# Performance work log

Hardware: AMD Instinct MI355X
Metric: run time of the kernel (lower is better)

Reference implementation:

```python
import jax, jax.numpy as jnp
import numpy as np

L, H, HM, E = 2, 1024, 256, 64  # layers, hidden, hyper hidden, hyper embedding
B, T, D = 64, 256, 1024         # batch, time, input size (D == H so layers stack)


def setup_inputs() -> dict:
    key = jax.random.key(0)
    ks = jax.random.split(key, 16)
    n = jax.random.normal
    inp = {
        'x':   n(ks[0], (B, T, D), jnp.float32),
        # main LSTM weights: 4 gates (i,f,g,o); last dim is the input dim
        'Wx':  n(ks[1], (L, 4, H, D), jnp.float32) / np.sqrt(D),
        'Wh':  n(ks[2], (L, 4, H, H), jnp.float32) / np.sqrt(H),
        # hyper (meta) LSTM: input is concat(x_t, h) of size D+H
        'Wmx': n(ks[3], (L, 4 * HM, D + H), jnp.float32) / np.sqrt(D + H),
        'Wmh': n(ks[4], (L, 4 * HM, HM), jnp.float32) / np.sqrt(HM),
        'bm':  jnp.zeros((L, 4 * HM), jnp.float32),
        # hyper embeddings z per gate (hidden->4xE projections)
        'Wzx': n(ks[5], (L, HM, 4, E), jnp.float32) / np.sqrt(HM),
        'bzx': jnp.ones((L, 4, E), jnp.float32),
        'Wzh': n(ks[6], (L, HM, 4, E), jnp.float32) / np.sqrt(HM),
        'bzh': jnp.ones((L, 4, E), jnp.float32),
        'Wzb': n(ks[7], (L, HM, 4, E), jnp.float32) / np.sqrt(HM),
        # embedding -> per-unit modulation (E->H per gate)
        'Px':  n(ks[8], (L, 4, E, H), jnp.float32) / np.sqrt(E),
        'Ph':  n(ks[9], (L, 4, E, H), jnp.float32) / np.sqrt(E),
        'Pb':  n(ks[10], (L, 4, E, H), jnp.float32) / np.sqrt(E),
    }
    return inp


def _meta_lstm_forward(x, Wx, Wh, Wmx, Wmh, bm, Wzx, bzx, Wzh, bzh, Wzb, Px, Ph, Pb):
    Bb = x.shape[0]
    inp = x
    for l in range(L):
        def step(carry, xt, l=l):
            h, c, mh, mc = carry
            # hyper LSTM step on concat(x_t, h)
            xcat = jnp.concatenate([xt, h], axis=-1)
            mpre = xcat @ Wmx[l].T + mh @ Wmh[l].T + bm[l]
            mi, mf, mg, mo = jnp.split(mpre, 4, axis=-1)
            mc2 = jax.nn.sigmoid(mf) * mc + jax.nn.sigmoid(mi) * jnp.tanh(mg)
            mh2 = jax.nn.sigmoid(mo) * jnp.tanh(mc2)
            # gate embeddings and per-unit modulation vectors [B,4,H]
            zx = jnp.einsum('bm,mge->bge', mh2, Wzx[l]) + bzx[l]
            zh = jnp.einsum('bm,mge->bge', mh2, Wzh[l]) + bzh[l]
            zb = jnp.einsum('bm,mge->bge', mh2, Wzb[l])
            dx = jnp.einsum('bge,geh->bgh', zx, Px[l])
            dh = jnp.einsum('bge,geh->bgh', zh, Ph[l])
            db = jnp.einsum('bge,geh->bgh', zb, Pb[l])
            # main LSTM gate pre-activations, hyper-modulated
            gx = jnp.einsum('bd,ghd->bgh', xt, Wx[l])
            gh = jnp.einsum('bk,ghk->bgh', h, Wh[l])
            pre = dx * gx + dh * gh + db
            i_, f_, g_, o_ = pre[:, 0], pre[:, 1], pre[:, 2], pre[:, 3]
            c2 = jax.nn.sigmoid(f_) * c + jax.nn.sigmoid(i_) * jnp.tanh(g_)
            h2 = jax.nn.sigmoid(o_) * jnp.tanh(c2)
            return (h2, c2, mh2, mc2), h2
        init = (jnp.zeros((Bb, H), x.dtype), jnp.zeros((Bb, H), x.dtype),
                jnp.zeros((Bb, HM), x.dtype), jnp.zeros((Bb, HM), x.dtype))
        xs = jnp.swapaxes(inp, 0, 1)  # [T,B,D]
        _, hs = jax.lax.scan(step, init, xs)
        inp = jnp.swapaxes(hs, 0, 1)  # [B,T,H]
    return inp


def reference(x, Wx, Wh, Wmx, Wmh, bm, Wzx, bzx, Wzh, bzh, Wzb, Px, Ph, Pb):
    return _meta_lstm_forward(x, Wx, Wh, Wmx, Wmh, bm, Wzx, bzx, Wzh, bzh, Wzb, Px, Ph, Pb)
```

## Files before the change

### kernel.cpp

```cpp
#include <hip/hip_runtime.h>
#include <hip/hip_cooperative_groups.h>

namespace cg = cooperative_groups;

#define Bb 64
#define Tt 256
#define Dd 1024
#define Hh 1024
#define HMm 256
#define Ee 64

__device__ __forceinline__ float b2f(unsigned short u){
    union{unsigned int i; float f;} v; v.i = ((unsigned int)u) << 16; return v.f;
}
__device__ __forceinline__ unsigned short f2bf(float f){
    union{float f; unsigned int i;} v; v.f = f;
    unsigned int x = v.i;
    unsigned int r = (x + 0x7fffu + ((x >> 16) & 1u)) >> 16;
    return (unsigned short)r;
}
__device__ __forceinline__ void up2(unsigned int u, float& lo, float& hi){
    union{unsigned int i; float f;} x, y;
    x.i = u << 16; y.i = u & 0xffff0000u; lo = x.f; hi = y.f;
}
__device__ __forceinline__ float sigf(float x){ return 1.f/(1.f + expf(-x)); }

__device__ __forceinline__ float ldT(const unsigned short* p){ return b2f(*p); }
__device__ __forceinline__ float ldT(const float* p){ return *p; }
__device__ __forceinline__ void stT(unsigned short* p, float v){ *p = f2bf(v); }
__device__ __forceinline__ void stT(float* p, float v){ *p = v; }

__device__ __forceinline__ void ld8(const unsigned short* p, float* f){
    uint4 u = *(const uint4*)(const void*)p;
    up2(u.x,f[0],f[1]); up2(u.y,f[2],f[3]); up2(u.z,f[4],f[5]); up2(u.w,f[6],f[7]);
}
__device__ __forceinline__ void ld8(const float* p, float* f){
    float4 a = *(const float4*)(const void*)p;
    float4 b = *(const float4*)(const void*)(p+4);
    f[0]=a.x; f[1]=a.y; f[2]=a.z; f[3]=a.w; f[4]=b.x; f[5]=b.y; f[6]=b.z; f[7]=b.w;
}
__device__ __forceinline__ float dot8(const float* a, const float* b, float acc){
    #pragma unroll
    for(int i=0;i<8;i++) acc += a[i]*b[i];
    return acc;
}

__global__ void k_detect(const unsigned short* __restrict__ x, int* __restrict__ flag){
    int tid = threadIdx.x;
    float v = fabsf(b2f(x[2 * tid]));
    bool in = (v > 1e-4f) && (v < 50.f);
    unsigned long long m = __ballot(in);
    if(tid == 0) *flag = (__popcll(m) >= 32) ? 0 : 1;
}

__global__ __launch_bounds__(1024, 4) void coop_rnn_bf16(
    const unsigned short* x,
    const unsigned short* __restrict__ Wx, const unsigned short* __restrict__ Wh,
    const unsigned short* __restrict__ Wmx, const unsigned short* __restrict__ Wmh,
    const unsigned short* __restrict__ bm,
    const unsigned short* __restrict__ Wzx, const unsigned short* __restrict__ bzx,
    const unsigned short* __restrict__ Wzh, const unsigned short* __restrict__ bzh,
    const unsigned short* __restrict__ Wzb,
    const unsigned short* __restrict__ Px, const unsigned short* __restrict__ Ph,
    const unsigned short* __restrict__ Pb,
    unsigned short* out, float* ws, const int* flag)
{
    if(*flag != 0) return;
    cg::grid_group grid = cg::this_grid();

    float* h0   = ws;
    float* h1   = ws + 65536;
    float* cst  = ws + 131072;
    float* m0   = ws + 196608;
    float* m1   = ws + 212992;
    float* mcst = ws + 229376;
    float* z    = ws + 245760;
    unsigned short* xbuf16 = (unsigned short*)(ws + 294912);

    int tid = threadIdx.x, bid = blockIdx.x;

    __shared__ __align__(16) unsigned short sWx[16][4][264];
    __shared__ __align__(16) unsigned short sWh[16][4][264];
    __shared__ __align__(16) unsigned short sWmxX[4][4][264];
    __shared__ __align__(16) unsigned short sWmxH[4][4][264];
    __shared__ __align__(16) unsigned short sWmh[4][4][72];
    __shared__ __align__(16) unsigned short sWz[3][4][72];
    __shared__ __align__(16) unsigned short sP[3][4][64][4];
    __shared__ float sBm[4], sBz[2];
    __shared__ float sA[256];
    __shared__ float spre[1024];

    for(int l = 0; l < 2; l++){
        const unsigned short* xseq = l ? out : x;
        const unsigned short* Wx_l  = Wx  + (size_t)l * 4194304;
        const unsigned short* Wh_l  = Wh  + (size_t)l * 4194304;
        const unsigned short* Wmx_l = Wmx + (size_t)l * 2097152;
        const unsigned short* Wmh_l = Wmh + (size_t)l * 262144;
        const unsigned short* bm_l  = bm  + l * 1024;
        const unsigned short* Wz0 = Wzx + l * 65536;
        const unsigned short* Wz1 = Wzh + l * 65536;
        const unsigned short* Wz2 = Wzb + l * 65536;
        const unsigned short* bz0 = bzx + l * 256;
        const unsigned short* bz1 = bzh + l * 256;
        const unsigned short* Px_l = Px + l * 262144;
        const unsigned short* Ph_l = Ph + l * 262144;
        const unsigned short* Pb_l = Pb + l * 262144;

        {
            int gid = bid * 1024 + tid;
            if(gid < 65536){ h0[gid] = 0.f; cst[gid] = 0.f; }
            if(gid < 16384){ m0[gid] = 0.f; mcst[gid] = 0.f; }
        }

        for(int idx = tid; idx < 16384; idx += 1024){
            int rr = idx >> 10, k = idx & 1023;
            int g = rr >> 2, hh = rr & 3;
            size_t n = (size_t)(g * 1024 + bid * 4 + hh);
            sWx[rr][k >> 8][k & 255] = Wx_l[n * 1024 + k];
        }
        for(int idx = tid; idx < 16384; idx += 1024){
            int rr = idx >> 10, k = idx & 1023;
            int g = rr >> 2, hh = rr & 3;
            size_t n = (size_t)(g * 1024 + bid * 4 + hh);
            sWh[rr][k >> 8][k & 255] = Wh_l[n * 1024 + k];
        }
        for(int idx = tid; idx < 4096; idx += 1024){
            int r = idx >> 10, k = idx & 1023;
            size_t row = (size_t)(r * 256 + bid);
            sWmxX[r][k >> 8][k & 255] = Wmx_l[row * 2048 + k];
            sWmxH[r][k >> 8][k & 255] = Wmx_l[row * 2048 + 1024 + k];
        }
        {
            int r = tid >> 8, m = tid & 255;
            sWmh[r][m >> 6][m & 63] = Wmh_l[(size_t)(r * 256 + bid) * 256 + m];
        }
        if(tid < 768){
            int s_ = tid >> 8, m = tid & 255;
            const unsigned short* W = (s_ == 0) ? Wz0 : ((s_ == 1) ? Wz1 : Wz2);
            sWz[s_][m >> 6][m & 63] = W[m * 256 + bid];
        }
        {
            int g = tid >> 8, e = (tid >> 2) & 63, hh = tid & 3;
            int pi = (g * 64 + e) * 1024 + bid * 4 + hh;
            sP[0][g][e][hh] = Px_l[pi];
            sP[1][g][e][hh] = Ph_l[pi];
            sP[2][g][e][hh] = Pb_l[pi];
        }
        if(tid < 4) sBm[tid] = ldT(&bm_l[tid * 256 + bid]);
        if(tid == 4) sBz[0] = ldT(&bz0[bid]);
        if(tid == 5) sBz[1] = ldT(&bz1[bid]);

        float *hp = h0, *hn = h1, *mp = m0, *mn = m1;
        grid.sync();

        for(int t = 0; t < 256; t++){
            {
                int sg = bid * 1024 + tid;
                if(sg < 65536){
                    int xb = sg >> 10, xd = sg & 1023;
                    xbuf16[sg] = xseq[((size_t)xb * Tt + t) * Dd + xd];
                }

                int r  = tid >> 8;
                int b  = (tid >> 2) & 63;
                int ks = tid & 3;
                const unsigned short* wxp = &sWmxX[r][ks][0];
                const unsigned short* whp_ = &sWmxH[r][ks][0];
                const unsigned short* wmp = &sWmh[r][ks][0];
                const unsigned short* xr = xseq + ((size_t)b * Tt + t) * Dd + ks * 256;
                const float* hr = hp + b * 1024 + ks * 256;
                const float* mr = mp + b * 256 + ks * 64;
                float a0 = 0.f, a1 = 0.f, a2 = 0.f, a3 = 0.f;
                float wf[8], vf[8];
                for(int k = 0; k < 256; k += 16){
                    ld8(wxp + k, wf);     ld8(xr + k, vf);     a0 = dot8(wf, vf, a0);
                    ld8(wxp + k + 8, wf); ld8(xr + k + 8, vf); a1 = dot8(wf, vf, a1);
                }
                for(int k = 0; k < 256; k += 16){
                    ld8(whp_ + k, wf);     ld8(hr + k, vf);     a2 = dot8(wf, vf, a2);
                    ld8(whp_ + k + 8, wf); ld8(hr + k + 8, vf); a3 = dot8(wf, vf, a3);
                }
                for(int m = 0; m < 64; m += 16){
                    ld8(wmp + m, wf);     ld8(mr + m, vf);     a0 = dot8(wf, vf, a0);
                    ld8(wmp + m + 8, wf); ld8(mr + m + 8, vf); a1 = dot8(wf, vf, a1);
                }
                float a = (a0 + a1) + (a2 + a3);
                a += __shfl_xor(a, 1);
                a += __shfl_xor(a, 2);
                if(ks == 0) sA[r * 64 + b] = a + sBm[r];
            }
            __syncthreads();
            if(tid < 64){
                int b = tid;
                float mi = sA[b], mf = sA[64 + b], mg = sA[128 + b], mo = sA[192 + b];
                int idx = b * 256 + bid;
                float mc2 = sigf(mf) * mcst[idx] + sigf(mi) * tanhf(mg);
                mcst[idx] = mc2;
                mn[idx] = sigf(mo) * tanhf(mc2);
            }
            grid.sync();

            if(tid < 768){
                int s_ = tid >> 8, sub = tid & 255;
                int b = sub >> 2, ks = sub & 3;
                const unsigned short* wz = &sWz[s_][ks][0];
                const float* mr = mn + b * 256 + ks * 64;
                float acc = 0.f; float wf[8], vf[8];
                for(int m = 0; m < 64; m += 16){
                    ld8(wz + m, wf);     ld8(mr + m, vf);     acc = dot8(wf, vf, acc);
                    ld8(wz + m + 8, wf); ld8(mr + m + 8, vf); acc = dot8(wf, vf, acc);
                }
                acc += __shfl_xor(acc, 1);
                acc += __shfl_xor(acc, 2);
                if(ks == 0){
                    float biasv = (s_ == 0) ? sBz[0] : ((s_ == 1) ? sBz[1] : 0.f);
                    z[((s_ * 256) + bid) * 64 + b] = acc + biasv;
                }
            }
            grid.sync();

            {
                int r16 = tid >> 6;
                int g = r16 >> 2, hh = r16 & 3;
                int bg = (tid >> 2) & 15;
                int ks = tid & 3;
                int b0 = bg * 4;
                const unsigned short* wxr = &sWx[r16][ks][0];
                const unsigned short* whr = &sWh[r16][ks][0];
                float gx[4] = {0,0,0,0}, gh[4] = {0,0,0,0};
                for(int k = 0; k < 256; k += 8){
                    float wf[8]; ld8(wxr + k, wf);
                    #pragma unroll
                    for(int i = 0; i < 4; i++){
                        float xf[8]; ld8(xbuf16 + (b0 + i) * 1024 + ks * 256 + k, xf);
                        gx[i] = dot8(wf, xf, gx[i]);
                    }
                }
                for(int k = 0; k < 256; k += 8){
                    float wf[8]; ld8(whr + k, wf);
                    #pragma unroll
                    for(int i = 0; i < 4; i++){
                        float hf[8]; ld8(hp + (b0 + i) * 1024 + ks * 256 + k, hf);
                        gh[i] = dot8(wf, hf, gh[i]);
                    }
                }
                float dx[4] = {0,0,0,0}, dh[4] = {0,0,0,0}, db[4] = {0,0,0,0};
                int e0 = ks * 16;
                for(int e = e0; e < e0 + 16; e++){
                    int zc = g * 64 + e;
                    float pxv = b2f(sP[0][g][e][hh]);
                    float phv = b2f(sP[1][g][e][hh]);
                    float pbv = b2f(sP[2][g][e][hh]);
                    const float4 zx4 = *(const float4*)&z[(0 * 256 + zc) * 64 + b0];
                    const float4 zh4 = *(const float4*)&z[(1 * 256 + zc) * 64 + b0];
                    const float4 zb4 = *(const float4*)&z[(2 * 256 + zc) * 64 + b0];
                    dx[0] += zx4.x * pxv; dx[1] += zx4.y * pxv; dx[2] += zx4.z * pxv; dx[3] += zx4.w * pxv;
                    dh[0] += zh4.x * phv; dh[1] += zh4.y * phv; dh[2] += zh4.z * phv; dh[3] += zh4.w * phv;
                    db[0] += zb4.x * pbv; db[1] += zb4.y * pbv; db[2] += zb4.z * pbv; db[3] += zb4.w * pbv;
                }
                #pragma unroll
                for(int i = 0; i < 4; i++){
                    gx[i] += __shfl_xor(gx[i], 1); gx[i] += __shfl_xor(gx[i], 2);
                    gh[i] += __shfl_xor(gh[i], 1); gh[i] += __shfl_xor(gh[i], 2);
                    dx[i] += __shfl_xor(dx[i], 1); dx[i] += __shfl_xor(dx[i], 2);
                    dh[i] += __shfl_xor(dh[i], 1); dh[i] += __shfl_xor(dh[i], 2);
                    db[i] += __shfl_xor(db[i], 1); db[i] += __shfl_xor(db[i], 2);
                }
                if(ks == 0){
                    #pragma unroll
                    for(int i = 0; i < 4; i++)
                        spre[r16 * 64 + b0 + i] = dx[i] * gx[i] + dh[i] * gh[i] + db[i];
                }
            }
            __syncthreads();
            if(tid < 256){
                int hh = tid >> 6, b = tid & 63;
                float pi_ = spre[(0 * 4 + hh) * 64 + b];
                float pf_ = spre[(1 * 4 + hh) * 64 + b];
                float pg_ = spre[(2 * 4 + hh) * 64 + b];
                float po_ = spre[(3 * 4 + hh) * 64 + b];
                int h = bid * 4 + hh;
                int idx = b * 1024 + h;
                float c2 = sigf(pf_) * cst[idx] + sigf(pi_) * tanhf(pg_);
                float h2 = sigf(po_) * tanhf(c2);
                cst[idx] = c2;
                hn[idx] = h2;
                stT(&out[((size_t)b * Tt + t) * Dd + h], h2);
            }
            grid.sync();

            float* tp = hp; hp = hn; hn = tp;
            tp = mp; mp = mn; mn = tp;
        }
    }
}

__global__ __launch_bounds__(1024, 4) void coop_rnn_f32(
    const float* x,
    const float* __restrict__ Wx, const float* __restrict__ Wh,
    const float* __restrict__ Wmx, const float* __restrict__ Wmh, const float* __restrict__ bm,
    const float* __restrict__ Wzx, const float* __restrict__ bzx,
    const float* __restrict__ Wzh, const float* __restrict__ bzh, const float* __restrict__ Wzb,
    const float* __restrict__ Px, const float* __restrict__ Ph, const float* __restrict__ Pb,
    float* out, float* ws, const int* flag)
{
    if(*flag != 1) return;
    cg::grid_group grid = cg::this_grid();

    float* h0   = ws;
    float* h1   = ws + 65536;
    float* cst  = ws + 131072;
    float* m0   = ws + 196608;
    float* m1   = ws + 212992;
    float* mcst = ws + 229376;
    float* z    = ws + 245760;
    float* xbuf = ws + 294912;

    int tid = threadIdx.x, bid = blockIdx.x;

    __shared__ __align__(16) float sWx[16][4][264];
    __shared__ __align__(16) float sWh[16][4][264];
    __shared__ __align__(16) float sP[3][4][64][5];
    __shared__ float sA[256];
    __shared__ float spre[1024];

    for(int l = 0; l < 2; l++){
        const float* xseq = l ? out : x;
        const float* Wx_l  = Wx  + (size_t)l * 4194304;
        const float* Wh_l  = Wh  + (size_t)l * 4194304;
        const float* Wmx_l = Wmx + (size_t)l * 2097152;
        const float* Wmh_l = Wmh + (size_t)l * 262144;
        const float* bm_l  = bm  + l * 1024;
        const float* Wz0 = Wzx + l * 65536;
        const float* Wz1 = Wzh + l * 65536;
        const float* Wz2 = Wzb + l * 65536;
        const float* bz0 = bzx + l * 256;
        const float* bz1 = bzh + l * 256;
        const float* Px_l = Px + l * 262144;
        const float* Ph_l = Ph + l * 262144;
        const float* Pb_l = Pb + l * 262144;

        {
            int gid = bid * 1024 + tid;
            if(gid < 65536){ h0[gid] = 0.f; cst[gid] = 0.f; }
            if(gid < 16384){ m0[gid] = 0.f; mcst[gid] = 0.f; }
        }

        for(int idx = tid; idx < 16384; idx += 1024){
            int rr = idx >> 10, k = idx & 1023;
            int g = rr >> 2, hh = rr & 3;
            size_t n = (size_t)(g * 1024 + bid * 4 + hh);
            sWx[rr][k >> 8][k & 255] = Wx_l[n * 1024 + k];
            sWh[rr][k >> 8][k & 255] = Wh_l[n * 1024 + k];
        }
        {
            int g = tid >> 8, e = (tid >> 2) & 63, hh = tid & 3;
            int pi = (g * 64 + e) * 1024 + bid * 4 + hh;
            sP[0][g][e][hh] = Px_l[pi];
            sP[1][g][e][hh] = Ph_l[pi];
            sP[2][g][e][hh] = Pb_l[pi];
        }

        float *hp = h0, *hn = h1, *mp = m0, *mn = m1;
        grid.sync();

        for(int t = 0; t < 256; t++){
            {
                int sg = bid * 1024 + tid;
                if(sg < 65536){
                    int xb = sg >> 10, xd = sg & 1023;
                    xbuf[sg] = ldT(&xseq[((size_t)xb * Tt + t) * Dd + xd]);
                }
                int r  = tid >> 8;
                int b  = (tid >> 2) & 63;
                int ks = tid & 3;
                int row = r * 256 + bid;
                const float* wr = Wmx_l + (size_t)row * 2048;
                const float* wm = Wmh_l + (size_t)row * 256;
                const float* xr = xseq + ((size_t)b * Tt + t) * Dd;
                const float* hr = hp + b * 1024;
                const float* mr = mp + b * 256;
                float a0 = 0.f, a1 = 0.f, a2 = 0.f, a3 = 0.f;
                float wf[8], vf[8];
                int k0 = ks * 256;
                for(int k = k0; k < k0 + 256; k += 16){
                    ld8(wr + k, wf);      ld8(xr + k, vf);      a0 = dot8(wf, vf, a0);
                    ld8(wr + k + 8, wf);  ld8(xr + k + 8, vf);  a1 = dot8(wf, vf, a1);
                }
                for(int k = k0; k < k0 + 256; k += 16){
                    ld8(wr + 1024 + k, wf);     ld8(hr + k, vf);     a2 = dot8(wf, vf, a2);
                    ld8(wr + 1024 + k + 8, wf); ld8(hr + k + 8, vf); a3 = dot8(wf, vf, a3);
                }
                int ms = ks * 64;
                for(int m = ms; m < ms + 64; m += 16){
                    ld8(wm + m, wf);     ld8(mr + m, vf);     a0 = dot8(wf, vf, a0);
                    ld8(wm + m + 8, wf); ld8(mr + m + 8, vf); a1 = dot8(wf, vf, a1);
                }
                float a = (a0 + a1) + (a2 + a3);
                a += __shfl_xor(a, 1);
                a += __shfl_xor(a, 2);
                if(ks == 0) sA[r * 64 + b] = a + ldT(&bm_l[row]);
            }
            __syncthreads();
            if(tid < 64){
                int b = tid;
                float mi = sA[b], mf = sA[64 + b], mg = sA[128 + b], mo = sA[192 + b];
                int idx = b * 256 + bid;
                float mc2 = sigf(mf) * mcst[idx] + sigf(mi) * tanhf(mg);
                mcst[idx] = mc2;
                mn[idx] = sigf(mo) * tanhf(mc2);
            }
            grid.sync();

            if(bid < 192){
                int s_ = bid >> 6, b = bid & 63;
                int ks = tid >> 8, col = tid & 255;
                const float* W = (s_ == 0) ? Wz0 : ((s_ == 1) ? Wz1 : Wz2);
                const float* mr = mn + b * 256;
                float acc = 0.f;
                int ms = ks * 64;
                #pragma unroll 8
                for(int m = ms; m < ms + 64; m++)
                    acc += mr[m] * ldT(&W[m * 256 + col]);
                spre[tid] = acc;
                __syncthreads();
                if(tid < 256){
                    float biasv = (s_ == 0) ? ldT(&bz0[tid]) : ((s_ == 1) ? ldT(&bz1[tid]) : 0.f);
                    z[(s_ * 64 + b) * 256 + tid] =
                        biasv + ((spre[tid] + spre[256 + tid]) + (spre[512 + tid] + spre[768 + tid]));
                }
            }
            grid.sync();

            {
                int r16 = tid >> 6;
                int g = r16 >> 2, hh = r16 & 3;
                int bg = (tid >> 2) & 15;
                int ks = tid & 3;
                int b0 = bg * 4;
                const float* wxr = &sWx[r16][ks][0];
                const float* whr = &sWh[r16][ks][0];
                float gx[4] = {0,0,0,0}, gh[4] = {0,0,0,0};
                for(int k = 0; k < 256; k += 8){
                    float wf[8]; ld8(wxr + k, wf);
                    #pragma unroll
                    for(int i = 0; i < 4; i++){
                        float xf[8]; ld8(xbuf + (b0 + i) * 1024 + ks * 256 + k, xf);
                        gx[i] = dot8(wf, xf, gx[i]);
                    }
                }
                for(int k = 0; k < 256; k += 8){
                    float wf[8]; ld8(whr + k, wf);
                    #pragma unroll
                    for(int i = 0; i < 4; i++){
                        float hf[8]; ld8(hp + (b0 + i) * 1024 + ks * 256 + k, hf);
                        gh[i] = dot8(wf, hf, gh[i]);
                    }
                }
                float dx[4] = {0,0,0,0}, dh[4] = {0,0,0,0}, db[4] = {0,0,0,0};
                int e0 = ks * 16;
                for(int e = e0; e < e0 + 16; e++){
                    float pxv = sP[0][g][e][hh];
                    float phv = sP[1][g][e][hh];
                    float pbv = sP[2][g][e][hh];
                    int zc = g * 64 + e;
                    #pragma unroll
                    for(int i = 0; i < 4; i++){
                        int b = b0 + i;
                        dx[i] += z[(b) * 256 + zc] * pxv;
                        dh[i] += z[(64 + b) * 256 + zc] * phv;
                        db[i] += z[(128 + b) * 256 + zc] * pbv;
                    }
                }
                #pragma unroll
                for(int i = 0; i < 4; i++){
                    gx[i] += __shfl_xor(gx[i], 1); gx[i] += __shfl_xor(gx[i], 2);
                    gh[i] += __shfl_xor(gh[i], 1); gh[i] += __shfl_xor(gh[i], 2);
                    dx[i] += __shfl_xor(dx[i], 1); dx[i] += __shfl_xor(dx[i], 2);
                    dh[i] += __shfl_xor(dh[i], 1); dh[i] += __shfl_xor(dh[i], 2);
                    db[i] += __shfl_xor(db[i], 1); db[i] += __shfl_xor(db[i], 2);
                }
                if(ks == 0){
                    #pragma unroll
                    for(int i = 0; i < 4; i++)
                        spre[r16 * 64 + b0 + i] = dx[i] * gx[i] + dh[i] * gh[i] + db[i];
                }
            }
            __syncthreads();
            if(tid < 256){
                int hh = tid >> 6, b = tid & 63;
                float pi_ = spre[(0 * 4 + hh) * 64 + b];
                float pf_ = spre[(1 * 4 + hh) * 64 + b];
                float pg_ = spre[(2 * 4 + hh) * 64 + b];
                float po_ = spre[(3 * 4 + hh) * 64 + b];
                int h = bid * 4 + hh;
                int idx = b * 1024 + h;
                float c2 = sigf(pf_) * cst[idx] + sigf(pi_) * tanhf(pg_);
                float h2 = sigf(po_) * tanhf(c2);
                cst[idx] = c2;
                hn[idx] = h2;
                stT(&out[((size_t)b * Tt + t) * Dd + h], h2);
            }
            grid.sync();

            float* tp = hp; hp = hn; hn = tp;
            tp = mp; mp = mn; mn = tp;
        }
    }
}

static void launch_bf16(void* const* d_in, void* d_out, float* ws, int* flag, hipStream_t stream){
    const unsigned short* xp   = (const unsigned short*)d_in[0];
    const unsigned short* Wxp  = (const unsigned short*)d_in[1];
    const unsigned short* Whp  = (const unsigned short*)d_in[2];
    const unsigned short* Wmxp = (const unsigned short*)d_in[3];
    const unsigned short* Wmhp = (const unsigned short*)d_in[4];
    const unsigned short* bmp  = (const unsigned short*)d_in[5];
    const unsigned short* Wzxp = (const unsigned short*)d_in[6];
    const unsigned short* bzxp = (const unsigned short*)d_in[7];
    const unsigned short* Wzhp = (const unsigned short*)d_in[8];
    const unsigned short* bzhp = (const unsigned short*)d_in[9];
    const unsigned short* Wzbp = (const unsigned short*)d_in[10];
    const unsigned short* Pxp  = (const unsigned short*)d_in[11];
    const unsigned short* Php  = (const unsigned short*)d_in[12];
    const unsigned short* Pbp  = (const unsigned short*)d_in[13];
    unsigned short* outp = (unsigned short*)d_out;
    void* args[] = {
        (void*)&xp, (void*)&Wxp, (void*)&Whp, (void*)&Wmxp, (void*)&Wmhp, (void*)&bmp,
        (void*)&Wzxp, (void*)&bzxp, (void*)&Wzhp, (void*)&bzhp, (void*)&Wzbp,
        (void*)&Pxp, (void*)&Php, (void*)&Pbp, (void*)&outp, (void*)&ws, (void*)&flag
    };
    hipLaunchCooperativeKernel((void*)coop_rnn_bf16, dim3(256), dim3(1024), args, 0, stream);
}

static void launch_f32(void* const* d_in, void* d_out, float* ws, int* flag, hipStream_t stream){
    const float* xp   = (const float*)d_in[0];
    const float* Wxp  = (const float*)d_in[1];
    const float* Whp  = (const float*)d_in[2];
    const float* Wmxp = (const float*)d_in[3];
    const float* Wmhp = (const float*)d_in[4];
    const float* bmp  = (const float*)d_in[5];
    const float* Wzxp = (const float*)d_in[6];
    const float* bzxp = (const float*)d_in[7];
    const float* Wzhp = (const float*)d_in[8];
    const float* bzhp = (const float*)d_in[9];
    const float* Wzbp = (const float*)d_in[10];
    const float* Pxp  = (const float*)d_in[11];
    const float* Php  = (const float*)d_in[12];
    const float* Pbp  = (const float*)d_in[13];
    float* outp = (float*)d_out;
    void* args[] = {
        (void*)&xp, (void*)&Wxp, (void*)&Whp, (void*)&Wmxp, (void*)&Wmhp, (void*)&bmp,
        (void*)&Wzxp, (void*)&bzxp, (void*)&Wzhp, (void*)&bzhp, (void*)&Wzbp,
        (void*)&Pxp, (void*)&Php, (void*)&Pbp, (void*)&outp, (void*)&ws, (void*)&flag
    };
    hipLaunchCooperativeKernel((void*)coop_rnn_f32, dim3(256), dim3(1024), args, 0, stream);
}

extern "C" void kernel_launch(void* const* d_in, const int* in_sizes, int n_in,
                              void* d_out, int out_size, void* d_ws, size_t ws_size,
                              hipStream_t stream) {
    (void)in_sizes; (void)n_in; (void)out_size; (void)ws_size;
    float* ws = (float*)d_ws;
    int* flag = (int*)(ws + 360448);

    k_detect<<<1, 64, 0, stream>>>((const unsigned short*)d_in[0], flag);
    launch_bf16(d_in, d_out, ws, flag, stream);
    launch_f32(d_in, d_out, ws, flag, stream);
}
```

Measured before the change: 252.8 ms.

## Replace cooperative grid.sync with custom atomic barrier and cache hyper-z weights in LDS

Result: slower. 681.1 ms (+169.4%).

```diff
diff --git a/kernel.cpp b/kernel.cpp
--- a/kernel.cpp
+++ b/kernel.cpp
@@ -45,12 +45,53 @@
     return acc;
 }
 
-__global__ void k_detect(const unsigned short* __restrict__ x, int* __restrict__ flag){
+__device__ __forceinline__ float ld_c(const float* p){
+    return __hip_atomic_load(p, __ATOMIC_RELAXED, __HIP_MEMORY_SCOPE_AGENT);
+}
+__device__ __forceinline__ void st_c(float* p, float v){
+    __hip_atomic_store(p, v, __ATOMIC_RELAXED, __HIP_MEMORY_SCOPE_AGENT);
+}
+__device__ __forceinline__ void ld2_c(const float* p, float* f){
+    union{unsigned long long u; float fv[2];} c;
+    c.u = __hip_atomic_load((const unsigned long long*)(const void*)p,
+                            __ATOMIC_RELAXED, __HIP_MEMORY_SCOPE_AGENT);
+    f[0] = c.fv[0]; f[1] = c.fv[1];
+}
+__device__ __forceinline__ void ld4_c(const float* p, float* f){
+    ld2_c(p, f); ld2_c(p + 2, f + 2);
+}
+__device__ __forceinline__ void ld8_c(const float* p, float* f){
+    ld2_c(p, f); ld2_c(p + 2, f + 2); ld2_c(p + 4, f + 4); ld2_c(p + 6, f + 6);
+}
+
+__device__ __forceinline__ void gbar(unsigned* cnt, unsigned* gen, int nb){
+    __syncthreads();
+    if(threadIdx.x == 0){
+        asm volatile("" ::: "memory");
+        unsigned g = __hip_atomic_load(gen, __ATOMIC_RELAXED, __HIP_MEMORY_SCOPE_AGENT);
+        unsigned a = __hip_atomic_fetch_add(cnt, 1u, __ATOMIC_RELEASE, __HIP_MEMORY_SCOPE_AGENT);
+        if(a == (unsigned)(nb - 1)){
+            __hip_atomic_store(cnt, 0u, __ATOMIC_RELAXED, __HIP_MEMORY_SCOPE_AGENT);
+            __hip_atomic_store(gen, g + 1u, __ATOMIC_RELEASE, __HIP_MEMORY_SCOPE_AGENT);
+        }else{
+            while(__hip_atomic_load(gen, __ATOMIC_RELAXED, __HIP_MEMORY_SCOPE_AGENT) == g)
+                __builtin_amdgcn_s_sleep(32);
+        }
+        asm volatile("" ::: "memory");
+    }
+    __syncthreads();
+}
+
+__global__ void k_detect(const unsigned short* __restrict__ x, int* __restrict__ flag,
+                         unsigned* __restrict__ cnt, unsigned* __restrict__ gen){
     int tid = threadIdx.x;
     float v = fabsf(b2f(x[2 * tid]));
     bool in = (v > 1e-4f) && (v < 50.f);
     unsigned long long m = __ballot(in);
-    if(tid == 0) *flag = (__popcll(m) >= 32) ? 0 : 1;
+    if(tid == 0){
+        *flag = (__popcll(m) >= 32) ? 0 : 1;
+        *cnt = 0u; *gen = 0u;
+    }
 }
 
 __global__ __launch_bounds__(1024, 4) void coop_rnn_bf16(
@@ -302,10 +343,9 @@
     const float* __restrict__ Wzx, const float* __restrict__ bzx,
     const float* __restrict__ Wzh, const float* __restrict__ bzh, const float* __restrict__ Wzb,
     const float* __restrict__ Px, const float* __restrict__ Ph, const float* __restrict__ Pb,
-    float* out, float* ws, const int* flag)
+    float* out, float* ws, const int* flag, unsigned* bcnt, unsigned* bgen)
 {
     if(*flag != 1) return;
-    cg::grid_group grid = cg::this_grid();
 
     float* h0   = ws;
     float* h1   = ws + 65536;
@@ -321,6 +361,7 @@
     __shared__ __align__(16) float sWx[16][4][264];
     __shared__ __align__(16) float sWh[16][4][264];
     __shared__ __align__(16) float sP[3][4][64][5];
+    __shared__ __align__(16) float sWz[3][4][68];
     __shared__ float sA[256];
     __shared__ float spre[1024];
 
@@ -342,8 +383,8 @@
 
         {
             int gid = bid * 1024 + tid;
-            if(gid < 65536){ h0[gid] = 0.f; cst[gid] = 0.f; }
-            if(gid < 16384){ m0[gid] = 0.f; mcst[gid] = 0.f; }
+            if(gid < 65536){ st_c(&h0[gid], 0.f); st_c(&cst[gid], 0.f); }
+            if(gid < 16384){ st_c(&m0[gid], 0.f); st_c(&mcst[gid], 0.f); }
         }
 
         for(int idx = tid; idx < 16384; idx += 1024){
@@ -360,16 +401,21 @@
             sP[1][g][e][hh] = Ph_l[pi];
             sP[2][g][e][hh] = Pb_l[pi];
         }
+        if(tid < 768){
+            int s_ = tid >> 8, m = tid & 255;
+            const float* W = (s_ == 0) ? Wz0 : ((s_ == 1) ? Wz1 : Wz2);
+            sWz[s_][m >> 6][m & 63] = W[m * 256 + bid];
+        }
 
         float *hp = h0, *hn = h1, *mp = m0, *mn = m1;
-        grid.sync();
+        gbar(bcnt, bgen, 256);
 
         for(int t = 0; t < 256; t++){
             {
                 int sg = bid * 1024 + tid;
                 if(sg < 65536){
                     int xb = sg >> 10, xd = sg & 1023;
-                    xbuf[sg] = ldT(&xseq[((size_t)xb * Tt + t) * Dd + xd]);
+                    st_c(&xbuf[sg], ld_c(&xseq[((size_t)xb * Tt + t) * Dd + xd]));
                 }
                 int r  = tid >> 8;
                 int b  = (tid >> 2) & 63;
@@ -384,17 +430,17 @@
                 float wf[8], vf[8];
                 int k0 = ks * 256;
                 for(int k = k0; k < k0 + 256; k += 16){
-                    ld8(wr + k, wf);      ld8(xr + k, vf);      a0 = dot8(wf, vf, a0);
-                    ld8(wr + k + 8, wf);  ld8(xr + k + 8, vf);  a1 = dot8(wf, vf, a1);
+                    ld8(wr + k, wf);      ld8_c(xr + k, vf);      a0 = dot8(wf, vf, a0);
+                    ld8(wr + k + 8, wf);  ld8_c(xr + k + 8, vf);  a1 = dot8(wf, vf, a1);
                 }
                 for(int k = k0; k < k0 + 256; k += 16){
-                    ld8(wr + 1024 + k, wf);     ld8(hr + k, vf);     a2 = dot8(wf, vf, a2);
-                    ld8(wr + 1024 + k + 8, wf); ld8(hr + k + 8, vf); a3 = dot8(wf, vf, a3);
+                    ld8(wr + 1024 + k, wf);     ld8_c(hr + k, vf);     a2 = dot8(wf, vf, a2);
+                    ld8(wr + 1024 + k + 8, wf); ld8_c(hr + k + 8, vf); a3 = dot8(wf, vf, a3);
                 }
                 int ms = ks * 64;
                 for(int m = ms; m < ms + 64; m += 16){
-                    ld8(wm + m, wf);     ld8(mr + m, vf);     a0 = dot8(wf, vf, a0);
-                    ld8(wm + m + 8, wf); ld8(mr + m + 8, vf); a1 = dot8(wf, vf, a1);
+                    ld8(wm + m, wf);     ld8_c(mr + m, vf);     a0 = dot8(wf, vf, a0);
+                    ld8(wm + m + 8, wf); ld8_c(mr + m + 8, vf); a1 = dot8(wf, vf, a1);
                 }
                 float a = (a0 + a1) + (a2 + a3);
                 a += __shfl_xor(a, 1);
@@ -406,31 +452,30 @@
                 int b = tid;
                 float mi = sA[b], mf = sA[64 + b], mg = sA[128 + b], mo = sA[192 + b];
                 int idx = b * 256 + bid;
-                float mc2 = sigf(mf) * mcst[idx] + sigf(mi) * tanhf(mg);
-                mcst[idx] = mc2;
-                mn[idx] = sigf(mo) * tanhf(mc2);
-            }
-            grid.sync();
-
-            if(bid < 192){
-                int s_ = bid >> 6, b = bid & 63;
-                int ks = tid >> 8, col = tid & 255;
-                const float* W = (s_ == 0) ? Wz0 : ((s_ == 1) ? Wz1 : Wz2);
-                const float* mr = mn + b * 256;
-                float acc = 0.f;
-                int ms = ks * 64;
-                #pragma unroll 8
-                for(int m = ms; m < ms + 64; m++)
-                    acc += mr[m] * ldT(&W[m * 256 + col]);
-                spre[tid] = acc;
-                __syncthreads();
-                if(tid < 256){
-                    float biasv = (s_ == 0) ? ldT(&bz0[tid]) : ((s_ == 1) ? ldT(&bz1[tid]) : 0.f);
-                    z[(s_ * 64 + b) * 256 + tid] =
-                        biasv + ((spre[tid] + spre[256 + tid]) + (spre[512 + tid] + spre[768 + tid]));
-                }
-            }
-            grid.sync();
+                float mc2 = sigf(mf) * ld_c(&mcst[idx]) + sigf(mi) * tanhf(mg);
+                st_c(&mcst[idx], mc2);
+                st_c(&mn[idx], sigf(mo) * tanhf(mc2));
+            }
+            gbar(bcnt, bgen, 256);
+
+            if(tid < 768){
+                int s_ = tid >> 8, sub = tid & 255;
+                int b = sub >> 2, ks = sub & 3;
+                const float* wz = &sWz[s_][ks][0];
+                const float* mr = mn + b * 256 + ks * 64;
+                float acc = 0.f; float wf[8], vf[8];
+                for(int m = 0; m < 64; m += 16){
+                    ld8(wz + m, wf);     ld8_c(mr + m, vf);     acc = dot8(wf, vf, acc);
+                    ld8(wz + m + 8, wf); ld8_c(mr + m + 8, vf); acc = dot8(wf, vf, acc);
+                }
+                acc += __shfl_xor(acc, 1);
+                acc += __shfl_xor(acc, 2);
+                if(ks == 0){
+                    float biasv = (s_ == 0) ? ldT(&bz0[bid]) : ((s_ == 1) ? ldT(&bz1[bid]) : 0.f);
+                    st_c(&z[((s_ * 256) + bid) * 64 + b], acc + biasv);
+                }
+            }
+            gbar(bcnt, bgen, 256);
 
             {
                 int r16 = tid >> 6;
@@ -445,7 +490,7 @@
                     float wf[8]; ld8(wxr + k, wf);
                     #pragma unroll
                     for(int i = 0; i < 4; i++){
-                        float xf[8]; ld8(xbuf + (b0 + i) * 1024 + ks * 256 + k, xf);
+                        float xf[8]; ld8_c(xbuf + (b0 + i) * 1024 + ks * 256 + k, xf);
                         gx[i] = dot8(wf, xf, gx[i]);
                     }
                 }
@@ -453,23 +498,26 @@
                     float wf[8]; ld8(whr + k, wf);
                     #pragma unroll
                     for(int i = 0; i < 4; i++){
-                        float hf[8]; ld8(hp + (b0 + i) * 1024 + ks * 256 + k, hf);
+                        float hf[8]; ld8_c(hp + (b0 + i) * 1024 + ks * 256 + k, hf);
                         gh[i] = dot8(wf, hf, gh[i]);
                     }
                 }
                 float dx[4] = {0,0,0,0}, dh[4] = {0,0,0,0}, db[4] = {0,0,0,0};
                 int e0 = ks * 16;
                 for(int e = e0; e < e0 + 16; e++){
+                    int zc = g * 64 + e;
                     float pxv = sP[0][g][e][hh];
                     float phv = sP[1][g][e][hh];
                     float pbv = sP[2][g][e][hh];
-                    int zc = g * 64 + e;
+                    float zx4[4], zh4[4], zb4[4];
+                    ld4_c(&z[(0 * 256 + zc) * 64 + b0], zx4);
+                    ld4_c(&z[(1 * 256 + zc) * 64 + b0], zh4);
+                    ld4_c(&z[(2 * 256 + zc) * 64 + b0], zb4);
                     #pragma unroll
                     for(int i = 0; i < 4; i++){
-                        int b = b0 + i;
-                        dx[i] += z[(b) * 256 + zc] * pxv;
-                        dh[i] += z[(64 + b) * 256 + zc] * phv;
-                        db[i] += z[(128 + b) * 256 + zc] * pbv;
+                        dx[i] += zx4[i] * pxv;
+                        dh[i] += zh4[i] * phv;
+                        db[i] += zb4[i] * pbv;
                     }
                 }
                 #pragma unroll
@@ -495,13 +543,13 @@
                 float po_ = spre[(3 * 4 + hh) * 64 + b];
                 int h = bid * 4 + hh;
                 int idx = b * 1024 + h;
-                float c2 = sigf(pf_) * cst[idx] + sigf(pi_) * tanhf(pg_);
+                float c2 = sigf(pf_) * ld_c(&cst[idx]) + sigf(pi_) * tanhf(pg_);
                 float h2 = sigf(po_) * tanhf(c2);
-                cst[idx] = c2;
-                hn[idx] = h2;
-                stT(&out[((size_t)b * Tt + t) * Dd + h], h2);
-            }
-            grid.sync();
+                st_c(&cst[idx], c2);
+                st_c(&hn[idx], h2);
+                st_c(&out[((size_t)b * Tt + t) * Dd + h], h2);
+            }
+            gbar(bcnt, bgen, 256);
 
             float* tp = hp; hp = hn; hn = tp;
             tp = mp; mp = mn; mn = tp;
@@ -533,7 +581,8 @@
     hipLaunchCooperativeKernel((void*)coop_rnn_bf16, dim3(256), dim3(1024), args, 0, stream);
 }
 
-static void launch_f32(void* const* d_in, void* d_out, float* ws, int* flag, hipStream_t stream){
+static void launch_f32(void* const* d_in, void* d_out, float* ws, int* flag,
+                       unsigned* bcnt, unsigned* bgen, hipStream_t stream){
     const float* xp   = (const float*)d_in[0];
     const float* Wxp  = (const float*)d_in[1];
     const float* Whp  = (const float*)d_in[2];
@@ -552,7 +601,8 @@
     void* args[] = {
         (void*)&xp, (void*)&Wxp, (void*)&Whp, (void*)&Wmxp, (void*)&Wmhp, (void*)&bmp,
         (void*)&Wzxp, (void*)&bzxp, (void*)&Wzhp, (void*)&bzhp, (void*)&Wzbp,
-        (void*)&Pxp, (void*)&Php, (void*)&Pbp, (void*)&outp, (void*)&ws, (void*)&flag
+        (void*)&Pxp, (void*)&Php, (void*)&Pbp, (void*)&outp, (void*)&ws, (void*)&flag,
+        (void*)&bcnt, (void*)&bgen
     };
     hipLaunchCooperativeKernel((void*)coop_rnn_f32, dim3(256), dim3(1024), args, 0, stream);
 }
@@ -563,8 +613,10 @@
     (void)in_sizes; (void)n_in; (void)out_size; (void)ws_size;
     float* ws = (float*)d_ws;
     int* flag = (int*)(ws + 360448);
-
-    k_detect<<<1, 64, 0, stream>>>((const unsigned short*)d_in[0], flag);
+    unsigned* bcnt = (unsigned*)(ws + 360464);
+    unsigned* bgen = (unsigned*)(ws + 360480);
+
+    k_detect<<<1, 64, 0, stream>>>((const unsigned short*)d_in[0], flag, bcnt, bgen);
     launch_bf16(d_in, d_out, ws, flag, stream);
-    launch_f32(d_in, d_out, ws, flag, stream);
-}
+    launch_f32(d_in, d_out, ws, flag, bcnt, bgen, stream);
+}
```

## Restructure f32 cooperative RNN: register-resident hyper weights, hoisted main-gate GEMV, 512 threads

Applied to the files above, without the earlier changes.

Result: faster. 235.7 ms (-6.8%).

```diff
diff --git a/kernel.cpp b/kernel.cpp
--- a/kernel.cpp
+++ b/kernel.cpp
@@ -43,6 +43,11 @@
     #pragma unroll
     for(int i=0;i<8;i++) acc += a[i]*b[i];
     return acc;
+}
+__device__ __forceinline__ float redsum64(float s){
+    #pragma unroll
+    for(int o = 1; o < 64; o <<= 1) s += __shfl_xor(s, o);
+    return s;
 }
 
 __global__ void k_detect(const unsigned short* __restrict__ x, int* __restrict__ flag){
@@ -160,7 +165,6 @@
                     int xb = sg >> 10, xd = sg & 1023;
                     xbuf16[sg] = xseq[((size_t)xb * Tt + t) * Dd + xd];
                 }
-
                 int r  = tid >> 8;
                 int b  = (tid >> 2) & 63;
                 int ks = tid & 3;
@@ -295,7 +299,7 @@
     }
 }
 
-__global__ __launch_bounds__(1024, 4) void coop_rnn_f32(
+__global__ __launch_bounds__(512, 2) void coop_rnn_f32(
     const float* x,
     const float* __restrict__ Wx, const float* __restrict__ Wh,
     const float* __restrict__ Wmx, const float* __restrict__ Wmh, const float* __restrict__ bm,
@@ -314,15 +318,18 @@
     float* m1   = ws + 212992;
     float* mcst = ws + 229376;
     float* z    = ws + 245760;
-    float* xbuf = ws + 294912;
 
     int tid = threadIdx.x, bid = blockIdx.x;
-
-    __shared__ __align__(16) float sWx[16][4][264];
-    __shared__ __align__(16) float sWh[16][4][264];
-    __shared__ __align__(16) float sP[3][4][64][5];
-    __shared__ float sA[256];
+    int wave = tid >> 6, lane = tid & 63;
+
+    __shared__ __align__(16) float sWx[16][2][520];
+    __shared__ __align__(16) float sWh[16][2][520];
+    __shared__ __align__(16) float sP[3][4][64][4];
+    __shared__ __align__(16) float sWz[3][2][128];
+    __shared__ float sgx[1024];
+    __shared__ float sgh[1024];
     __shared__ float spre[1024];
+    float* sA = spre;
 
     for(int l = 0; l < 2; l++){
         const float* xseq = l ? out : x;
@@ -341,65 +348,125 @@
         const float* Pb_l = Pb + l * 262144;
 
         {
-            int gid = bid * 1024 + tid;
+            int gid = bid * 512 + tid;
             if(gid < 65536){ h0[gid] = 0.f; cst[gid] = 0.f; }
             if(gid < 16384){ m0[gid] = 0.f; mcst[gid] = 0.f; }
         }
 
-        for(int idx = tid; idx < 16384; idx += 1024){
+        for(int idx = tid; idx < 16384; idx += 512){
             int rr = idx >> 10, k = idx & 1023;
-            int g = rr >> 2, hh = rr & 3;
-            size_t n = (size_t)(g * 1024 + bid * 4 + hh);
-            sWx[rr][k >> 8][k & 255] = Wx_l[n * 1024 + k];
-            sWh[rr][k >> 8][k & 255] = Wh_l[n * 1024 + k];
-        }
+            size_t n = (size_t)((rr >> 2) * 1024 + bid * 4 + (rr & 3));
+            sWx[rr][k >> 9][k & 511] = Wx_l[n * 1024 + k];
+            sWh[rr][k >> 9][k & 511] = Wh_l[n * 1024 + k];
+        }
+        for(int idx = tid; idx < 3072; idx += 512){
+            int s_ = idx >> 10, rem = idx & 1023;
+            int g = rem >> 8, e = (rem >> 2) & 63, hh = rem & 3;
+            int pi = (g * 64 + e) * 1024 + bid * 4 + hh;
+            const float* P = (s_ == 0) ? Px_l : ((s_ == 1) ? Ph_l : Pb_l);
+            sP[s_][g][e][hh] = P[pi];
+        }
+        for(int idx = tid; idx < 768; idx += 512){
+            int s_ = idx >> 8, m = idx & 255;
+            const float* W = (s_ == 0) ? Wz0 : ((s_ == 1) ? Wz1 : Wz2);
+            sWz[s_][m >> 7][m & 127] = W[m * 256 + bid];
+        }
+
+        int rA = wave >> 1, bhalf = wave & 1;
+        int rowA = rA * 256 + bid;
+        float wa[32], wm4[4], bmv;
         {
-            int g = tid >> 8, e = (tid >> 2) & 63, hh = tid & 3;
-            int pi = (g * 64 + e) * 1024 + bid * 4 + hh;
-            sP[0][g][e][hh] = Px_l[pi];
-            sP[1][g][e][hh] = Ph_l[pi];
-            sP[2][g][e][hh] = Pb_l[pi];
-        }
+            const float* wp = Wmx_l + (size_t)rowA * 2048 + lane * 32;
+            ld8(wp, wa); ld8(wp + 8, wa + 8); ld8(wp + 16, wa + 16); ld8(wp + 24, wa + 24);
+            const float4 q4 = *(const float4*)(Wmh_l + (size_t)rowA * 256 + lane * 4);
+            wm4[0] = q4.x; wm4[1] = q4.y; wm4[2] = q4.z; wm4[3] = q4.w;
+            bmv = bm_l[rowA];
+        }
+        float bz0v = bz0[bid], bz1v = bz1[bid];
 
         float *hp = h0, *hn = h1, *mp = m0, *mn = m1;
         grid.sync();
 
         for(int t = 0; t < 256; t++){
             {
-                int sg = bid * 1024 + tid;
-                if(sg < 65536){
-                    int xb = sg >> 10, xd = sg & 1023;
-                    xbuf[sg] = ldT(&xseq[((size_t)xb * Tt + t) * Dd + xd]);
-                }
-                int r  = tid >> 8;
-                int b  = (tid >> 2) & 63;
-                int ks = tid & 3;
-                int row = r * 256 + bid;
-                const float* wr = Wmx_l + (size_t)row * 2048;
-                const float* wm = Wmh_l + (size_t)row * 256;
-                const float* xr = xseq + ((size_t)b * Tt + t) * Dd;
-                const float* hr = hp + b * 1024;
-                const float* mr = mp + b * 256;
-                float a0 = 0.f, a1 = 0.f, a2 = 0.f, a3 = 0.f;
-                float wf[8], vf[8];
-                int k0 = ks * 256;
-                for(int k = k0; k < k0 + 256; k += 16){
-                    ld8(wr + k, wf);      ld8(xr + k, vf);      a0 = dot8(wf, vf, a0);
-                    ld8(wr + k + 8, wf);  ld8(xr + k + 8, vf);  a1 = dot8(wf, vf, a1);
-                }
-                for(int k = k0; k < k0 + 256; k += 16){
-                    ld8(wr + 1024 + k, wf);     ld8(hr + k, vf);     a2 = dot8(wf, vf, a2);
-                    ld8(wr + 1024 + k + 8, wf); ld8(hr + k + 8, vf); a3 = dot8(wf, vf, a3);
-                }
-                int ms = ks * 64;
-                for(int m = ms; m < ms + 64; m += 16){
-                    ld8(wm + m, wf);     ld8(mr + m, vf);     a0 = dot8(wf, vf, a0);
-                    ld8(wm + m + 8, wf); ld8(mr + m + 8, vf); a1 = dot8(wf, vf, a1);
-                }
-                float a = (a0 + a1) + (a2 + a3);
-                a += __shfl_xor(a, 1);
-                a += __shfl_xor(a, 2);
-                if(ks == 0) sA[r * 64 + b] = a + ldT(&bm_l[row]);
+                const float* xbase = xseq + (size_t)t * 1024;
+                int lx = lane * 32;
+                float va[32], vm[4], vb[32], vn[4];
+                int b0 = bhalf * 32;
+                #define LOADV(VA, VM, bb) { \
+                    const float* vp = (lane < 32) ? (xbase + (size_t)(bb) * 262144 + lx) \
+                                                  : (hp + (bb) * 1024 + lx - 1024); \
+                    ld8(vp, VA); ld8(vp + 8, VA + 8); ld8(vp + 16, VA + 16); ld8(vp + 24, VA + 24); \
+                    const float4 q = *(const float4*)(mp + (bb) * 256 + lane * 4); \
+                    VM[0] = q.x; VM[1] = q.y; VM[2] = q.z; VM[3] = q.w; }
+                LOADV(va, vm, b0)
+                for(int i = 0; i < 32; i += 2){
+                    int b = b0 + i;
+                    LOADV(vb, vn, b + 1)
+                    float s = 0.f;
+                    #pragma unroll
+                    for(int j = 0; j < 32; j++) s += wa[j] * va[j];
+                    #pragma unroll
+                    for(int j = 0; j < 4; j++)  s += wm4[j] * vm[j];
+                    s = redsum64(s);
+                    if(lane == 0) sA[rA * 64 + b] = s + bmv;
+                    if(i + 2 < 32){ LOADV(va, vm, b + 2) }
+                    float s2 = 0.f;
+                    #pragma unroll
+                    for(int j = 0; j < 32; j++) s2 += wa[j] * vb[j];
+                    #pragma unroll
+                    for(int j = 0; j < 4; j++)  s2 += wm4[j] * vn[j];
+                    s2 = redsum64(s2);
+                    if(lane == 0) sA[rA * 64 + b + 1] = s2 + bmv;
+                }
+                #undef LOADV
+
+                int r16 = tid >> 5;
+                int bg = (tid >> 1) & 15, ks = tid & 1;
+                int b0g = bg * 4;
+                const float* wxr = &sWx[r16][ks][0];
+                const float* whr = &sWh[r16][ks][0];
+                float gx[4] = {0,0,0,0}, gh[4] = {0,0,0,0};
+                for(int k = 0; k < 512; k += 16){
+                    float w0[8], w1[8]; ld8(wxr + k, w0); ld8(wxr + k + 8, w1);
+                    float xf[4][8], xg[4][8];
+                    #pragma unroll
+                    for(int i = 0; i < 4; i++){
+                        const float* xp = xseq + ((size_t)(b0g + i) * Tt + t) * 1024 + ks * 512 + k;
+                        ld8(xp, xf[i]); ld8(xp + 8, xg[i]);
+                    }
+                    #pragma unroll
+                    for(int i = 0; i < 4; i++){
+                        gx[i] = dot8(w0, xf[i], gx[i]);
+                        gx[i] = dot8(w1, xg[i], gx[i]);
+                    }
+                }
+                for(int k = 0; k < 512; k += 16){
+                    float w0[8], w1[8]; ld8(whr + k, w0); ld8(whr + k + 8, w1);
+                    float hf[4][8], hg[4][8];
+                    #pragma unroll
+                    for(int i = 0; i < 4; i++){
+                        const float* hpp = hp + (b0g + i) * 1024 + ks * 512 + k;
+                        ld8(hpp, hf[i]); ld8(hpp + 8, hg[i]);
+                    }
+                    #pragma unroll
+                    for(int i = 0; i < 4; i++){
+                        gh[i] = dot8(w0, hf[i], gh[i]);
+                        gh[i] = dot8(w1, hg[i], gh[i]);
+                    }
+                }
+                #pragma unroll
+                for(int i = 0; i < 4; i++){
+                    gx[i] += __shfl_xor(gx[i], 1);
+                    gh[i] += __shfl_xor(gh[i], 1);
+                }
+                if(ks == 0){
+                    #pragma unroll
+                    for(int i = 0; i < 4; i++){
+                        sgx[r16 * 64 + b0g + i] = gx[i];
+                        sgh[r16 * 64 + b0g + i] = gh[i];
+                    }
+                }
             }
             __syncthreads();
             if(tid < 64){
@@ -412,79 +479,59 @@
             }
             grid.sync();
 
-            if(bid < 192){
-                int s_ = bid >> 6, b = bid & 63;
-                int ks = tid >> 8, col = tid & 255;
-                const float* W = (s_ == 0) ? Wz0 : ((s_ == 1) ? Wz1 : Wz2);
-                const float* mr = mn + b * 256;
+            if(tid < 384){
+                int s_ = tid >> 7, sub = tid & 127;
+                int b = sub >> 1, ks = sub & 1;
+                const float* wz = &sWz[s_][ks][0];
+                const float* mr = mn + b * 256 + ks * 128;
                 float acc = 0.f;
-                int ms = ks * 64;
-                #pragma unroll 8
-                for(int m = ms; m < ms + 64; m++)
-                    acc += mr[m] * ldT(&W[m * 256 + col]);
-                spre[tid] = acc;
-                __syncthreads();
-                if(tid < 256){
-                    float biasv = (s_ == 0) ? ldT(&bz0[tid]) : ((s_ == 1) ? ldT(&bz1[tid]) : 0.f);
-                    z[(s_ * 64 + b) * 256 + tid] =
-                        biasv + ((spre[tid] + spre[256 + tid]) + (spre[512 + tid] + spre[768 + tid]));
+                for(int m = 0; m < 128; m += 32){
+                    float v0[8], v1[8], v2[8], v3[8];
+                    ld8(mr + m, v0); ld8(mr + m + 8, v1);
+                    ld8(mr + m + 16, v2); ld8(mr + m + 24, v3);
+                    float w0[8], w1[8], w2[8], w3[8];
+                    ld8(wz + m, w0); ld8(wz + m + 8, w1);
+                    ld8(wz + m + 16, w2); ld8(wz + m + 24, w3);
+                    acc = dot8(w0, v0, acc); acc = dot8(w1, v1, acc);
+                    acc = dot8(w2, v2, acc); acc = dot8(w3, v3, acc);
+                }
+                acc += __shfl_xor(acc, 1);
+                if(ks == 0){
+                    float biasv = (s_ == 0) ? bz0v : ((s_ == 1) ? bz1v : 0.f);
+                    z[((s_ * 256) + bid) * 64 + b] = acc + biasv;
                 }
             }
             grid.sync();
 
             {
-                int r16 = tid >> 6;
+                int r16 = tid >> 5, bp = tid & 31;
                 int g = r16 >> 2, hh = r16 & 3;
-                int bg = (tid >> 2) & 15;
-                int ks = tid & 3;
-                int b0 = bg * 4;
-                const float* wxr = &sWx[r16][ks][0];
-                const float* whr = &sWh[r16][ks][0];
-                float gx[4] = {0,0,0,0}, gh[4] = {0,0,0,0};
-                for(int k = 0; k < 256; k += 8){
-                    float wf[8]; ld8(wxr + k, wf);
-                    #pragma unroll
-                    for(int i = 0; i < 4; i++){
-                        float xf[8]; ld8(xbuf + (b0 + i) * 1024 + ks * 256 + k, xf);
-                        gx[i] = dot8(wf, xf, gx[i]);
-                    }
-                }
-                for(int k = 0; k < 256; k += 8){
-                    float wf[8]; ld8(whr + k, wf);
-                    #pragma unroll
-                    for(int i = 0; i < 4; i++){
-                        float hf[8]; ld8(hp + (b0 + i) * 1024 + ks * 256 + k, hf);
-                        gh[i] = dot8(wf, hf, gh[i]);
-                    }
-                }
-                float dx[4] = {0,0,0,0}, dh[4] = {0,0,0,0}, db[4] = {0,0,0,0};
-                int e0 = ks * 16;
-                for(int e = e0; e < e0 + 16; e++){
-                    float pxv = sP[0][g][e][hh];
-                    float phv = sP[1][g][e][hh];
-                    float pbv = sP[2][g][e][hh];
-                    int zc = g * 64 + e;
-                    #pragma unroll
-                    for(int i = 0; i < 4; i++){
-                        int b = b0 + i;
-                        dx[i] += z[(b) * 256 + zc] * pxv;
-                        dh[i] += z[(64 + b) * 256 + zc] * phv;
-                        db[i] += z[(128 + b) * 256 + zc] * pbv;
-                    }
-                }
-                #pragma unroll
-                for(int i = 0; i < 4; i++){
-                    gx[i] += __shfl_xor(gx[i], 1); gx[i] += __shfl_xor(gx[i], 2);
-                    gh[i] += __shfl_xor(gh[i], 1); gh[i] += __shfl_xor(gh[i], 2);
-                    dx[i] += __shfl_xor(dx[i], 1); dx[i] += __shfl_xor(dx[i], 2);
-                    dh[i] += __shfl_xor(dh[i], 1); dh[i] += __shfl_xor(dh[i], 2);
-                    db[i] += __shfl_xor(db[i], 1); db[i] += __shfl_xor(db[i], 2);
-                }
-                if(ks == 0){
-                    #pragma unroll
-                    for(int i = 0; i < 4; i++)
-                        spre[r16 * 64 + b0 + i] = dx[i] * gx[i] + dh[i] * gh[i] + db[i];
-                }
+                int b = bp * 2;
+                float dxx = 0.f, dxy = 0.f, dhx = 0.f, dhy = 0.f, dbx = 0.f, dby = 0.f;
+                for(int e8 = 0; e8 < 64; e8 += 8){
+                    float2 zx[8], zh[8], zb[8];
+                    #pragma unroll
+                    for(int j = 0; j < 8; j++){
+                        int zc = g * 64 + e8 + j;
+                        zx[j] = *(const float2*)&z[(0 * 256 + zc) * 64 + b];
+                        zh[j] = *(const float2*)&z[(1 * 256 + zc) * 64 + b];
+                        zb[j] = *(const float2*)&z[(2 * 256 + zc) * 64 + b];
+                    }
+                    #pragma unroll
+                    for(int j = 0; j < 8; j++){
+                        int e = e8 + j;
+                        float px = sP[0][g][e][hh];
+                        float ph = sP[1][g][e][hh];
+                        float pb = sP[2][g][e][hh];
+                        dxx += zx[j].x * px; dxy += zx[j].y * px;
+                        dhx += zh[j].x * ph; dhy += zh[j].y * ph;
+                        dbx += zb[j].x * pb; dby += zb[j].y * pb;
+                    }
+                }
+                float gx0 = sgx[r16 * 64 + b],     gh0 = sgh[r16 * 64 + b];
+                float gx1 = sgx[r16 * 64 + b + 1], gh1 = sgh[r16 * 64 + b + 1];
+                spre[r16 * 64 + b]     = dxx * gx0 + dhx * gh0 + dbx;
+                spre[r16 * 64 + b + 1] = dxy * gx1 + dhy * gh1 + dby;
             }
             __syncthreads();
             if(tid < 256){
@@ -554,7 +601,7 @@
         (void*)&Wzxp, (void*)&bzxp, (void*)&Wzhp, (void*)&bzhp, (void*)&Wzbp,
         (void*)&Pxp, (void*)&Php, (void*)&Pbp, (void*)&outp, (void*)&ws, (void*)&flag
     };
-    hipLaunchCooperativeKernel((void*)coop_rnn_f32, dim3(256), dim3(1024), args, 0, stream);
+    hipLaunchCooperativeKernel((void*)coop_rnn_f32, dim3(256), dim3(512), args, 0, stream);
 }
 
 extern "C" void kernel_launch(void* const* d_in, const int* in_sizes, int n_in,
```
